# Kernel optimization log

Hardware: AMD Instinct MI355X
Metric: run time of the kernel (lower is better)

## Reference

```python
import jax, jax.numpy as jnp
from jax import lax
import numpy as np

B, T, I, H, C = 32, 256, 128, 128, 100


def setup_inputs() -> dict:
    key = jax.random.key(0)
    ks = jax.random.split(key, 9)
    s = 1.0 / np.sqrt(H)  # PyTorch LSTMCell init range
    inp = {
        "x": jax.random.normal(ks[0], (B, T, I), dtype=jnp.float32),
        "w_ih": jax.random.uniform(ks[1], (4 * H, I), jnp.float32, -s, s),
        "b_ih": jax.random.uniform(ks[2], (4 * H,), jnp.float32, -s, s),
        "w_hh": jax.random.uniform(ks[3], (4 * H, H), jnp.float32, -s, s),
        "b_hh": jax.random.uniform(ks[4], (4 * H,), jnp.float32, -s, s),
        # attention params: normal(mean=0, std=0.01) per the source
        "w1": 0.01 * jax.random.normal(ks[5], (2 * H, H), dtype=jnp.float32),
        "w2": 0.01 * jax.random.normal(ks[6], (H, 1), dtype=jnp.float32),
        "w_fc": jax.random.uniform(ks[7], (C, H), jnp.float32, -s, s),
        "b_fc": jax.random.uniform(ks[8], (C,), jnp.float32, -s, s),
    }
    return inp


def _forward(x, w_ih, b_ih, w_hh, b_hh, w1, w2, w_fc, b_fc):
    Bv, Tv, _ = x.shape
    Hv = w_hh.shape[1]
    h0 = jnp.zeros((Bv, Hv), x.dtype)
    c0 = jnp.zeros((Bv, Hv), x.dtype)
    # memory buffer: slot 0 holds the initial zero hidden state (as in the
    # torch code, h_old starts as h_t=0); slots 1..T filled as we go.
    # Unwritten (future) slots are zero, so their attn contribution
    # attn_w * h_old is exactly zero -> no mask needed, matching the
    # growing-memory semantics of the original loop.
    mem0 = jnp.zeros((Bv, Tv + 1, Hv), x.dtype)
    attn0 = jnp.zeros((Bv, Hv), x.dtype)

    def step(carry, inp):
        h, c, mem, _ = carry
        x_t, i = inp
        # PyTorch LSTMCell: gate order i, f, g, o
        gates = x_t @ w_ih.T + b_ih + h @ w_hh.T + b_hh
        ig, fg, gg, og = jnp.split(gates, 4, axis=-1)
        c = jax.nn.sigmoid(fg) * c + jax.nn.sigmoid(ig) * jnp.tanh(gg)
        h = jax.nn.sigmoid(og) * jnp.tanh(c)
        # additive attention scores over the memory (NO softmax in source)
        h_rep = jnp.broadcast_to(h[:, None, :], mem.shape)  # [B, T+1, H]
        cat = jnp.concatenate([h_rep, mem], axis=-1)        # [B, T+1, 2H]
        s = jnp.tanh(cat @ w1) @ w2                          # [B, T+1, 1]
        attn_c = jnp.sum(s * mem, axis=1)                    # [B, H]
        mem = mem.at[:, i + 1, :].set(h)  # append h_t to memory
        return (h, c, mem, attn_c), None

    xs = (jnp.transpose(x, (1, 0, 2)), jnp.arange(Tv))
    (h, c, mem, attn_c), _ = lax.scan(step, (h0, c0, mem0, attn0), xs)
    return (h + attn_c) @ w_fc.T + b_fc


def reference(x, w_ih, b_ih, w_hh, b_hh, w1, w2, w_fc, b_fc):
    return _forward(x, w_ih, b_ih, w_hh, b_hh, w1, w2, w_fc, b_fc)
```

## Files before the change

kernel.cpp:

```cpp
#include <hip/hip_runtime.h>
#include <hip/hip_bf16.h>


#define Bsz 32
#define Tsz 256
#define Isz 128
#define Hsz 128
#define Csz 100
#define G4H 512

typedef short v8s __attribute__((ext_vector_type(8)));
typedef float v4fa __attribute__((ext_vector_type(4)));

__device__ __forceinline__ float quad_rsum(float x) {
    int t = __builtin_amdgcn_update_dpp(0, __float_as_int(x), 0xB1, 0xF, 0xF, true);
    x += __int_as_float(t);
    t = __builtin_amdgcn_update_dpp(0, __float_as_int(x), 0x4E, 0xF, 0xF, true);
    x += __int_as_float(t);
    return x;
}
__device__ __forceinline__ float rcpf(float x) { return __builtin_amdgcn_rcpf(x); }
__device__ __forceinline__ float ex2(float x) { return __builtin_amdgcn_exp2f(x); }
__device__ __forceinline__ float sigm_n(float x) {
    return rcpf(1.0f + ex2(-1.442695041f * x));
}
__device__ __forceinline__ float tanh_n(float x) {
    return fmaf(-2.0f, rcpf(1.0f + ex2(2.885390082f * x)), 1.0f);
}
__device__ __forceinline__ short bf16_bits(float x) {
    __hip_bfloat16 h = __float2bfloat16(x);
    return *reinterpret_cast<short*>(&h);
}
__device__ __forceinline__ float bf16_val(float x) {
    return __bfloat162float(__float2bfloat16(x));
}

__global__ __launch_bounds__(256) void prep_kernel(
    const float* __restrict__ w_ih, const float* __restrict__ b_ih,
    const float* __restrict__ w_hh, const float* __restrict__ b_hh,
    const float* __restrict__ w1,
    __hip_bfloat16* __restrict__ W2ih, __hip_bfloat16* __restrict__ W2v,
    float* __restrict__ whh_pk, float* __restrict__ bias,
    float* __restrict__ attn_c) {
    int idx = blockIdx.x * blockDim.x + threadIdx.x;
    if (idx < G4H * Isz) {
        int n = idx >> 7;
        int k = idx & 127;
        float x = w_ih[idx];
        __hip_bfloat16 hi = __float2bfloat16(x);
        __hip_bfloat16 lo = __float2bfloat16(x - __bfloat162float(hi));
        W2ih[(size_t)n * 384 + k] = hi;
        W2ih[(size_t)n * 384 + 128 + k] = lo;
        W2ih[(size_t)n * 384 + 256 + k] = hi;

        int j4  = idx & 3;
        int q   = (idx >> 2) & 3;
        int d   = (idx >> 4) & 127;
        int gi  = (idx >> 11) & 3;
        int kk4 = (idx >> 13) & 7;
        whh_pk[idx] = w_hh[(size_t)((gi << 7) + d) * 128 + (q << 5) + (kk4 << 2) + j4];
    }
    if (idx < Hsz * Hsz) {
        int n = idx >> 7;
        int k = idx & 127;
        float x = w1[(size_t)(128 + k) * Hsz + n];
        __hip_bfloat16 hi = __float2bfloat16(x);
        __hip_bfloat16 lo = __float2bfloat16(x - __bfloat162float(hi));
        W2v[(size_t)n * 384 + k] = hi;
        W2v[(size_t)n * 384 + 128 + k] = lo;
        W2v[(size_t)n * 384 + 256 + k] = hi;
    }
    if (idx < G4H) bias[idx] = b_ih[idx] + b_hh[idx];
    if (idx < Bsz * Hsz) attn_c[idx] = 0.0f;
}

__global__ __launch_bounds__(256) void gemm_mfma_f32a(
    const float* __restrict__ A, const __hip_bfloat16* __restrict__ W2,
    const float* __restrict__ bias, float* __restrict__ C, int M, int N) {
    const int tid = threadIdx.x;
    const int w = tid >> 6, lane = tid & 63;
    const int m0 = blockIdx.y * 64 + (w & 1) * 32;
    const int n0 = blockIdx.x * 64 + (w >> 1) * 32;
    const int r = lane & 15, quad = lane >> 4;

    v8s Ahi[2][4], Alo[2][4];
    #pragma unroll
    for (int i = 0; i < 2; ++i)
        #pragma unroll
        for (int cb = 0; cb < 4; ++cb) {
            const float* src = A + (size_t)(m0 + 16 * i + r) * Isz + cb * 32 + quad * 8;
            float4 f0 = *(const float4*)src;
            float4 f1 = *(const float4*)(src + 4);
            float f[8] = {f0.x, f0.y, f0.z, f0.w, f1.x, f1.y, f1.z, f1.w};
            v8s hi, lo;
            #pragma unroll
            for (int e = 0; e < 8; ++e) {
                float hv = bf16_val(f[e]);
                hi[e] = bf16_bits(f[e]);
                lo[e] = bf16_bits(f[e] - hv);
            }
            Ahi[i][cb] = hi;
            Alo[i][cb] = lo;
        }

    v4fa acc[2][2] = {};
    const short* Wb = (const short*)W2;
    #pragma unroll
    for (int ks = 0; ks < 12; ++ks) {
        int cb = ks & 3;
        v8s a0 = (ks >= 8) ? Alo[0][cb] : Ahi[0][cb];
        v8s a1 = (ks >= 8) ? Alo[1][cb] : Ahi[1][cb];
        int kb = ks * 32 + quad * 8;
        v8s b0 = *(const v8s*)(Wb + (size_t)(n0 + r) * 384 + kb);
        v8s b1 = *(const v8s*)(Wb + (size_t)(n0 + 16 + r) * 384 + kb);
        acc[0][0] = __builtin_amdgcn_mfma_f32_16x16x32_bf16(a0, b0, acc[0][0], 0, 0, 0);
        acc[0][1] = __builtin_amdgcn_mfma_f32_16x16x32_bf16(a0, b1, acc[0][1], 0, 0, 0);
        acc[1][0] = __builtin_amdgcn_mfma_f32_16x16x32_bf16(a1, b0, acc[1][0], 0, 0, 0);
        acc[1][1] = __builtin_amdgcn_mfma_f32_16x16x32_bf16(a1, b1, acc[1][1], 0, 0, 0);
    }
    #pragma unroll
    for (int i = 0; i < 2; ++i)
        #pragma unroll
        for (int j = 0; j < 2; ++j) {
            int cn = n0 + 16 * j + r;
            float bb = bias ? bias[cn] : 0.0f;
            #pragma unroll
            for (int rr = 0; rr < 4; ++rr) {
                int row = m0 + 16 * i + quad * 4 + rr;
                C[(size_t)row * N + cn] = acc[i][j][rr] + bb;
            }
        }
}

#define HPAD(k) ((k) + 8 * ((k) >> 5))

__global__ __launch_bounds__(512, 2) void lstm_seq(
    const float* __restrict__ G, const float* __restrict__ whh_pk,
    float* __restrict__ H_all) {
    const int b = blockIdx.x;
    const int tid = threadIdx.x;
    const int d = tid >> 2;
    const int q = tid & 3;

    __shared__ float h_s[2][160];

    float2 w2v[4][16];
    {
        const float4* wp = (const float4*)whh_pk;
        #pragma unroll
        for (int kk4 = 0; kk4 < 8; ++kk4)
            #pragma unroll
            for (int gi = 0; gi < 4; ++gi) {
                float4 v = wp[((kk4 * 4 + gi) * 128 + d) * 4 + q];
                w2v[gi][kk4 * 2]     = make_float2(v.x, v.y);
                w2v[gi][kk4 * 2 + 1] = make_float2(v.z, v.w);
            }
    }

    if (tid < 320) ((float*)h_s)[tid] = 0.0f;
    float c = 0.0f;
    __syncthreads();

    const float* Gq = G + (size_t)b * Tsz * G4H + q * 128 + d;
    float* Hst = H_all + (size_t)b * Tsz * Hsz + d;

    float gval = Gq[0];
    int cur = 0;
    for (int t = 0; t < Tsz; ++t) {
        const int tn = (t < Tsz - 1) ? t + 1 : t;
        float ngval = Gq[(size_t)tn * G4H];

        float2 accA[4], accB[4];
        #pragma unroll
        for (int gi = 0; gi < 4; ++gi) {
            accA[gi] = make_float2(q == gi ? gval : 0.f, 0.f);
            accB[gi] = make_float2(0.f, 0.f);
        }
        const float4* hb4 = (const float4*)&h_s[cur][q * 40];
        #pragma unroll
        for (int kk4 = 0; kk4 < 8; ++kk4) {
            float4 h4 = hb4[kk4];
            #pragma unroll
            for (int gi = 0; gi < 4; ++gi) {
                accA[gi].x = fmaf(h4.x, w2v[gi][2 * kk4].x, accA[gi].x);
                accA[gi].y = fmaf(h4.y, w2v[gi][2 * kk4].y, accA[gi].y);
                accB[gi].x = fmaf(h4.z, w2v[gi][2 * kk4 + 1].x, accB[gi].x);
                accB[gi].y = fmaf(h4.w, w2v[gi][2 * kk4 + 1].y, accB[gi].y);
            }
        }
        float a0 = quad_rsum(accA[0].x + accA[0].y + accB[0].x + accB[0].y);
        float a1 = quad_rsum(accA[1].x + accA[1].y + accB[1].x + accB[1].y);
        float a2 = quad_rsum(accA[2].x + accA[2].y + accB[2].x + accB[2].y);
        float a3 = quad_rsum(accA[3].x + accA[3].y + accB[3].x + accB[3].y);

        float iv = sigm_n(a0);
        float fv = sigm_n(a1);
        float gv = tanh_n(a2);
        float ov = sigm_n(a3);
        c = fmaf(fv, c, iv * gv);
        float h = ov * tanh_n(c);

        if (q == 0) {
            h_s[cur ^ 1][HPAD(d)] = h;
            Hst[(size_t)t * Hsz] = h;
        }
        gval = ngval;
        __builtin_amdgcn_sched_barrier(0);
        asm volatile("s_waitcnt lgkmcnt(0)" ::: "memory");
        __builtin_amdgcn_s_barrier();
        __builtin_amdgcn_sched_barrier(0);
        cur ^= 1;
    }
}

__global__ __launch_bounds__(256) void scores_part(
    const float* __restrict__ H_all, const float* __restrict__ KV,
    const float* __restrict__ w1, const float* __restrict__ w2,
    float* __restrict__ attn_c) {
    const int b = blockIdx.y, jt = blockIdx.x;
    const int tid = threadIdx.x;
    __shared__ float hT[Hsz];
    __shared__ float q_s[Hsz];
    __shared__ float w2s[Hsz];
    __shared__ float s_s[64];
    __shared__ float part[2][Hsz];

    const float* Hb = H_all + (size_t)b * Tsz * Hsz;
    const float* KVb = KV + (size_t)b * Tsz * Hsz;

    if (tid < Hsz) {
        hT[tid] = Hb[255 * Hsz + tid];
        w2s[tid] = w2[tid];
    }
    __syncthreads();
    if (tid < Hsz) {
        float acc = 0.f;
        #pragma unroll 8
        for (int k = 0; k < Hsz; ++k) acc = fmaf(hT[k], w1[k * Hsz + tid], acc);
        q_s[tid] = acc;
    }
    __syncthreads();

    const int jl = tid >> 2, ql = tid & 3;
    const int j = jt * 64 + jl;
    float p = 0.f;
    if (j < 255) {
        const float* kv = KVb + (size_t)j * Hsz + ql * 32;
        const float* qs = q_s + ql * 32;
        const float* wv = w2s + ql * 32;
        #pragma unroll 8
        for (int k = 0; k < 32; ++k)
            p = fmaf(tanh_n(qs[k] + kv[k]), wv[k], p);
    }
    p = quad_rsum(p);
    if (ql == 0) s_s[jl] = (j < 255) ? p : 0.0f;
    __syncthreads();

    {
        const int dd = tid & 127, half = tid >> 7;
        float acc = 0.f;
        #pragma unroll 4
        for (int u = 0; u < 32; ++u) {
            int lj = half * 32 + u;
            int jj = jt * 64 + lj;
            if (jj < 255) acc = fmaf(s_s[lj], Hb[(size_t)jj * Hsz + dd], acc);
        }
        part[half][dd] = acc;
    }
    __syncthreads();
    if (tid < Hsz) atomicAdd(&attn_c[b * Hsz + tid], part[0][tid] + part[1][tid]);
}

__global__ __launch_bounds__(256) void fc_out(
    const float* __restrict__ H_all, const float* __restrict__ attn_c,
    const float* __restrict__ w_fc, const float* __restrict__ b_fc,
    float* __restrict__ out) {
    const int b = blockIdx.x, tid = threadIdx.x;
    __shared__ float r_s[Hsz];
    if (tid < Hsz)
        r_s[tid] = H_all[(size_t)b * Tsz * Hsz + 255 * Hsz + tid] + attn_c[b * Hsz + tid];
    __syncthreads();
    const int o = tid >> 1, half = tid & 1;
    float acc = 0.f;
    if (o < Csz) {
        const float* wr = w_fc + (size_t)o * Hsz + half * 64;
        const float* rr = r_s + half * 64;
        #pragma unroll 8
        for (int k = 0; k < 64; ++k) acc = fmaf(rr[k], wr[k], acc);
    }
    acc += __shfl_xor(acc, 1);
    if (half == 0 && o < Csz) out[b * Csz + o] = acc + b_fc[o];
}

extern "C" void kernel_launch(void* const* d_in, const int* in_sizes, int n_in,
                              void* d_out, int out_size, void* d_ws, size_t ws_size,
                              hipStream_t stream) {
    const float* x    = (const float*)d_in[0];
    const float* w_ih = (const float*)d_in[1];
    const float* b_ih = (const float*)d_in[2];
    const float* w_hh = (const float*)d_in[3];
    const float* b_hh = (const float*)d_in[4];
    const float* w1   = (const float*)d_in[5];
    const float* w2   = (const float*)d_in[6];
    const float* w_fc = (const float*)d_in[7];
    const float* b_fc = (const float*)d_in[8];

    float* ws = (float*)d_ws;
    float* whh_pk = ws;
    float* bias   = whh_pk + 65536;
    float* attn_c = bias + 512;
    __hip_bfloat16* W2ih = (__hip_bfloat16*)(attn_c + 4096);
    __hip_bfloat16* W2v  = (__hip_bfloat16*)(attn_c + 4096 + 98304);
    float* G      = attn_c + 4096 + 98304 + 24576;
    float* H_all  = G + 4194304;
    float* KV     = H_all + 1048576;

    prep_kernel<<<256, 256, 0, stream>>>(w_ih, b_ih, w_hh, b_hh, w1,
                                         W2ih, W2v, whh_pk, bias, attn_c);

    dim3 gG(G4H / 64, (Bsz * Tsz) / 64);
    gemm_mfma_f32a<<<gG, 256, 0, stream>>>(x, W2ih, bias, G, Bsz * Tsz, G4H);

    lstm_seq<<<Bsz, 512, 0, stream>>>(G, whh_pk, H_all);

    dim3 gK(Hsz / 64, (Bsz * Tsz) / 64);
    gemm_mfma_f32a<<<gK, 256, 0, stream>>>(H_all, W2v, nullptr, KV, Bsz * Tsz, Hsz);

    dim3 gS(4, Bsz);
    scores_part<<<gS, 256, 0, stream>>>(H_all, KV, w1, w2, attn_c);

    fc_out<<<Bsz, 256, 0, stream>>>(H_all, attn_c, w_fc, b_fc, (float*)d_out);
}
```

Baseline: 363.2 us.

## Fuse KV projection GEMM into scores kernel and use packed FMA in LSTM

Removes the separate MFMA GEMM launch that wrote KV to global memory. The scores kernel now computes its 64-row KV tile in shared memory with split-bf16 MFMAs and reads it from there. The LSTM recurrence inner loop also switches to two-wide vector FMAs so the compiler can emit packed FMA instructions. The cost is a larger shared-memory footprint and redundant W2v loads in the scores kernel, which is tiny compared with the sequential LSTM.

```diff
diff --git a/kernel.cpp b/kernel.cpp
--- a/kernel.cpp
+++ b/kernel.cpp
@@ -11,7 +11,9 @@
 
 typedef short v8s __attribute__((ext_vector_type(8)));
 typedef float v4fa __attribute__((ext_vector_type(4)));
-
+typedef float v2f __attribute__((ext_vector_type(2)));
+
+__device__ __forceinline__ v2f mk2(float a, float b) { v2f r; r.x = a; r.y = b; return r; }
 __device__ __forceinline__ float quad_rsum(float x) {
     int t = __builtin_amdgcn_update_dpp(0, __float_as_int(x), 0xB1, 0xF, 0xF, true);
     x += __int_as_float(t);
@@ -144,7 +146,7 @@
 
     __shared__ float h_s[2][160];
 
-    float2 w2v[4][16];
+    v2f w2v[4][16];
     {
         const float4* wp = (const float4*)whh_pk;
         #pragma unroll
@@ -152,8 +154,8 @@
             #pragma unroll
             for (int gi = 0; gi < 4; ++gi) {
                 float4 v = wp[((kk4 * 4 + gi) * 128 + d) * 4 + q];
-                w2v[gi][kk4 * 2]     = make_float2(v.x, v.y);
-                w2v[gi][kk4 * 2 + 1] = make_float2(v.z, v.w);
+                w2v[gi][kk4 * 2]     = mk2(v.x, v.y);
+                w2v[gi][kk4 * 2 + 1] = mk2(v.z, v.w);
             }
     }
 
@@ -170,23 +172,26 @@
         const int tn = (t < Tsz - 1) ? t + 1 : t;
         float ngval = Gq[(size_t)tn * G4H];
 
-        float2 accA[4], accB[4];
+        v2f accA[4], accB[4];
         #pragma unroll
         for (int gi = 0; gi < 4; ++gi) {
-            accA[gi] = make_float2(q == gi ? gval : 0.f, 0.f);
-            accB[gi] = make_float2(0.f, 0.f);
+            accA[gi] = mk2(q == gi ? gval : 0.f, 0.f);
+            accB[gi] = mk2(0.f, 0.f);
         }
         const float4* hb4 = (const float4*)&h_s[cur][q * 40];
         #pragma unroll
         for (int kk4 = 0; kk4 < 8; ++kk4) {
             float4 h4 = hb4[kk4];
-            #pragma unroll
-            for (int gi = 0; gi < 4; ++gi) {
-                accA[gi].x = fmaf(h4.x, w2v[gi][2 * kk4].x, accA[gi].x);
-                accA[gi].y = fmaf(h4.y, w2v[gi][2 * kk4].y, accA[gi].y);
-                accB[gi].x = fmaf(h4.z, w2v[gi][2 * kk4 + 1].x, accB[gi].x);
-                accB[gi].y = fmaf(h4.w, w2v[gi][2 * kk4 + 1].y, accB[gi].y);
-            }
+            v2f hA = mk2(h4.x, h4.y);
+            v2f hB = mk2(h4.z, h4.w);
+            accA[0] = __builtin_elementwise_fma(hA, w2v[0][2 * kk4], accA[0]);
+            accA[1] = __builtin_elementwise_fma(hA, w2v[1][2 * kk4], accA[1]);
+            accA[2] = __builtin_elementwise_fma(hA, w2v[2][2 * kk4], accA[2]);
+            accA[3] = __builtin_elementwise_fma(hA, w2v[3][2 * kk4], accA[3]);
+            accB[0] = __builtin_elementwise_fma(hB, w2v[0][2 * kk4 + 1], accB[0]);
+            accB[1] = __builtin_elementwise_fma(hB, w2v[1][2 * kk4 + 1], accB[1]);
+            accB[2] = __builtin_elementwise_fma(hB, w2v[2][2 * kk4 + 1], accB[2]);
+            accB[3] = __builtin_elementwise_fma(hB, w2v[3][2 * kk4 + 1], accB[3]);
         }
         float a0 = quad_rsum(accA[0].x + accA[0].y + accB[0].x + accB[0].y);
         float a1 = quad_rsum(accA[1].x + accA[1].y + accB[1].x + accB[1].y);
@@ -213,12 +218,13 @@
     }
 }
 
-__global__ __launch_bounds__(256) void scores_part(
-    const float* __restrict__ H_all, const float* __restrict__ KV,
+__global__ __launch_bounds__(256) void kv_scores(
+    const float* __restrict__ H_all, const __hip_bfloat16* __restrict__ W2v,
     const float* __restrict__ w1, const float* __restrict__ w2,
     float* __restrict__ attn_c) {
-    const int b = blockIdx.y, jt = blockIdx.x;
+    const int b = blockIdx.x >> 2, jt = blockIdx.x & 3;
     const int tid = threadIdx.x;
+    __shared__ float kv_s[64][132];
     __shared__ float hT[Hsz];
     __shared__ float q_s[Hsz];
     __shared__ float w2s[Hsz];
@@ -226,13 +232,71 @@
     __shared__ float part[2][Hsz];
 
     const float* Hb = H_all + (size_t)b * Tsz * Hsz;
-    const float* KVb = KV + (size_t)b * Tsz * Hsz;
 
     if (tid < Hsz) {
         hT[tid] = Hb[255 * Hsz + tid];
         w2s[tid] = w2[tid];
     }
-    __syncthreads();
+
+    {
+        const int w = tid >> 6, lane = tid & 63;
+        const int m0 = (w & 1) * 32;
+        const int n0 = (w >> 1) * 32;
+        const int r = lane & 15, quad = lane >> 4;
+        const float* Abase = Hb + (size_t)(jt * 64) * Hsz;
+
+        v8s Ahi[2][4], Alo[2][4];
+        #pragma unroll
+        for (int i = 0; i < 2; ++i)
+            #pragma unroll
+            for (int cb = 0; cb < 4; ++cb) {
+                const float* src = Abase + (size_t)(m0 + 16 * i + r) * Hsz + cb * 32 + quad * 8;
+                float4 f0 = *(const float4*)src;
+                float4 f1 = *(const float4*)(src + 4);
+                float f[8] = {f0.x, f0.y, f0.z, f0.w, f1.x, f1.y, f1.z, f1.w};
+                v8s hi, lo;
+                #pragma unroll
+                for (int e = 0; e < 8; ++e) {
+                    float hv = bf16_val(f[e]);
+                    hi[e] = bf16_bits(f[e]);
+                    lo[e] = bf16_bits(f[e] - hv);
+                }
+                Ahi[i][cb] = hi;
+                Alo[i][cb] = lo;
+            }
+
+        v4fa acc[2][2][2] = {};
+        const short* Wb = (const short*)W2v;
+        #pragma unroll
+        for (int ks = 0; ks < 12; ++ks) {
+            int cb = ks & 3;
+            v8s a0 = (ks >= 8) ? Alo[0][cb] : Ahi[0][cb];
+            v8s a1 = (ks >= 8) ? Alo[1][cb] : Ahi[1][cb];
+            int kb = ks * 32 + quad * 8;
+            #pragma unroll
+            for (int nh = 0; nh < 2; ++nh) {
+                int nn = nh * 64 + n0;
+                v8s b0 = *(const v8s*)(Wb + (size_t)(nn + r) * 384 + kb);
+                v8s b1 = *(const v8s*)(Wb + (size_t)(nn + 16 + r) * 384 + kb);
+                acc[nh][0][0] = __builtin_amdgcn_mfma_f32_16x16x32_bf16(a0, b0, acc[nh][0][0], 0, 0, 0);
+                acc[nh][0][1] = __builtin_amdgcn_mfma_f32_16x16x32_bf16(a0, b1, acc[nh][0][1], 0, 0, 0);
+                acc[nh][1][0] = __builtin_amdgcn_mfma_f32_16x16x32_bf16(a1, b0, acc[nh][1][0], 0, 0, 0);
+                acc[nh][1][1] = __builtin_amdgcn_mfma_f32_16x16x32_bf16(a1, b1, acc[nh][1][1], 0, 0, 0);
+            }
+        }
+        #pragma unroll
+        for (int nh = 0; nh < 2; ++nh)
+            #pragma unroll
+            for (int i = 0; i < 2; ++i)
+                #pragma unroll
+                for (int j = 0; j < 2; ++j)
+                    #pragma unroll
+                    for (int rr = 0; rr < 4; ++rr)
+                        kv_s[m0 + 16 * i + quad * 4 + rr][nh * 64 + n0 + 16 * j + r] =
+                            acc[nh][i][j][rr];
+    }
+    __syncthreads();
+
     if (tid < Hsz) {
         float acc = 0.f;
         #pragma unroll 8
@@ -245,12 +309,11 @@
     const int j = jt * 64 + jl;
     float p = 0.f;
     if (j < 255) {
-        const float* kv = KVb + (size_t)j * Hsz + ql * 32;
-        const float* qs = q_s + ql * 32;
-        const float* wv = w2s + ql * 32;
         #pragma unroll 8
-        for (int k = 0; k < 32; ++k)
-            p = fmaf(tanh_n(qs[k] + kv[k]), wv[k], p);
+        for (int kk = 0; kk < 32; ++kk) {
+            int k = ql * 32 + ((kk + ql) & 31);
+            p = fmaf(tanh_n(q_s[k] + kv_s[jl][k]), w2s[k], p);
+        }
     }
     p = quad_rsum(p);
     if (ql == 0) s_s[jl] = (j < 255) ? p : 0.0f;
@@ -313,7 +376,6 @@
     __hip_bfloat16* W2v  = (__hip_bfloat16*)(attn_c + 4096 + 98304);
     float* G      = attn_c + 4096 + 98304 + 24576;
     float* H_all  = G + 4194304;
-    float* KV     = H_all + 1048576;
 
     prep_kernel<<<256, 256, 0, stream>>>(w_ih, b_ih, w_hh, b_hh, w1,
                                          W2ih, W2v, whh_pk, bias, attn_c);
@@ -323,11 +385,7 @@
 
     lstm_seq<<<Bsz, 512, 0, stream>>>(G, whh_pk, H_all);
 
-    dim3 gK(Hsz / 64, (Bsz * Tsz) / 64);
-    gemm_mfma_f32a<<<gK, 256, 0, stream>>>(H_all, W2v, nullptr, KV, Bsz * Tsz, Hsz);
-
-    dim3 gS(4, Bsz);
-    scores_part<<<gS, 256, 0, stream>>>(H_all, KV, w1, w2, attn_c);
+    kv_scores<<<Bsz * 4, 256, 0, stream>>>(H_all, W2v, w1, w2, attn_c);
 
     fc_out<<<Bsz, 256, 0, stream>>>(H_all, attn_c, w_fc, b_fc, (float*)d_out);
 }
```

Result: faster. 340.9 us (-6.1%).
